# Performance work log

Measured on AMD Instinct MI355X. Metric: run time of the kernel, lower is better.

The kernel has to match this reference:

```python
import jax, jax.numpy as jnp
import numpy as np

T = 256        # number of time steps (len(ts))
B = 4096       # batch of independent ODE trajectories
D = 64         # data_size (state dim)
W = 256        # width_size
DT = 0.01      # time step


def setup_inputs() -> dict:
    key = jax.random.key(0)
    ks = jax.random.split(key, 9)
    ts = jnp.arange(T, dtype=jnp.float32) * DT
    y0 = jax.random.normal(ks[0], (B, D), dtype=jnp.float32)
    # MLP params: layers D->W, W->W, W->W, W->D (depth=3 hidden layers)
    def lin(k, out_d, in_d):
        return jax.random.normal(k, (out_d, in_d), dtype=jnp.float32) / np.float32(np.sqrt(in_d))
    w0 = lin(ks[1], W, D)
    b0 = jax.random.normal(ks[2], (W,), dtype=jnp.float32) * 0.01
    w1 = lin(ks[3], W, W)
    b1 = jax.random.normal(ks[4], (W,), dtype=jnp.float32) * 0.01
    w2 = lin(ks[5], W, W)
    b2 = jax.random.normal(ks[6], (W,), dtype=jnp.float32) * 0.01
    w3 = lin(ks[7], D, W)
    b3 = jax.random.normal(ks[8], (D,), dtype=jnp.float32) * 0.01
    return {"ts": ts, "y0": y0, "w0": w0, "b0": b0, "w1": w1, "b1": b1,
            "w2": w2, "b2": b2, "w3": w3, "b3": b3}


def reference(ts, y0, w0, b0, w1, b1, w2, b2, w3, b3):
    def mlp(y):  # y: [B, D] -> [B, D], softplus hidden activations
        h = jax.nn.softplus(y @ w0.T + b0)
        h = jax.nn.softplus(h @ w1.T + b1)
        h = jax.nn.softplus(h @ w2.T + b2)
        return h @ w3.T + b3

    dt = ts[1] - ts[0]

    def step(y, _):
        k1 = mlp(y)
        # NOTE: faithful to source: perturbations are 0.5*k1 and 0.75*k2 (no dt factor)
        k2 = mlp(y + 0.5 * k1)
        k3 = mlp(y + 0.75 * k2)
        y1 = (2.0 / 9.0 * k1 + 1.0 / 3.0 * k2 + 4.0 / 9.0 * k3) * dt + y
        return y1, y1

    _, ys = jax.lax.scan(step, y0, xs=None, length=ts.shape[0])
    return ys  # [T, B, D]
```

## Files before the change

kernel.cpp:

```cpp
#include <hip/hip_runtime.h>
#include <stdint.h>
#include <stddef.h>

constexpr int T_STEPS  = 256;
constexpr int B_ROWS   = 4096;
constexpr int D_DIM    = 64;
constexpr int W_DIM    = 256;
constexpr int ROWS_PB  = 16;
constexpr int NTHREADS = 512;

typedef __attribute__((ext_vector_type(8))) __bf16 bf16x8;
typedef __attribute__((ext_vector_type(8))) short  short8;
typedef __attribute__((ext_vector_type(4))) float  f32x4;

__device__ __forceinline__ unsigned f2bf_bits(float f) {
    union { float f; unsigned u; } v; v.f = f;
    return (v.u + 0x7FFFu + ((v.u >> 16) & 1u)) >> 16;
}

__device__ __forceinline__ uint32_t cvt_pk_bf16(float lo, float hi) {
    uint32_t r;
    asm("v_cvt_pk_bf16_f32 %0, %1, %2" : "=v"(r) : "v"(lo), "v"(hi));
    return r;
}

__device__ __forceinline__ float softplus_f(float x) {
    float e = __builtin_amdgcn_exp2f(-fabsf(x) * 1.44269504f);
    float l = __builtin_amdgcn_logf(1.0f + e);
    return fmaxf(x, 0.0f) + 0.69314718f * l;
}

__device__ __forceinline__ bf16x8 load_wfrag(const float* __restrict__ wg, int ldk,
                                             int f, int kcbase, int lg) {
    short8 s;
#pragma unroll
    for (int j = 0; j < 8; ++j) {
        const int k = kcbase + lg * 4 + (j >> 1) + ((j & 1) << 4);
        s[j] = (short)f2bf_bits(wg[(size_t)f * ldk + k]);
    }
    return __builtin_bit_cast(bf16x8, s);
}

template<int NKC>
__device__ __forceinline__ void mlp_layer(const uint32_t* __restrict__ srow,
                                          uint32_t* __restrict__ dst,
                                          const bf16x8* wf0, const bf16x8* wf1,
                                          float b0v, float b1v,
                                          int lr, int lg, int fbdw)
{
    const int swz = (lr & 7) << 2;
    f32x4 a0 = {b0v, b0v, b0v, b0v};
    f32x4 a1 = {b1v, b1v, b1v, b1v};
#pragma unroll
    for (int kc = 0; kc < NKC; ++kc) {
        const bf16x8 a = *reinterpret_cast<const bf16x8*>(srow + ((kc * 16 + lg * 4) ^ swz));
        a0 = __builtin_amdgcn_mfma_f32_16x16x32_bf16(a, wf0[kc], a0, 0, 0, 0);
        a1 = __builtin_amdgcn_mfma_f32_16x16x32_bf16(a, wf1[kc], a1, 0, 0, 0);
    }
#pragma unroll
    for (int j = 0; j < 4; ++j) {
        const int r = lg * 4 + j;
        dst[(size_t)r * 128 + ((fbdw + lr) ^ ((r & 7) << 2))] =
            cvt_pk_bf16(softplus_f(a0[j]), softplus_f(a1[j]));
    }
}

__global__ __launch_bounds__(NTHREADS, 2) void node_rk3_kernel(
    const float* __restrict__ ts,
    const float* __restrict__ y0,
    const float* __restrict__ w0, const float* __restrict__ b0,
    const float* __restrict__ w1, const float* __restrict__ b1,
    const float* __restrict__ w2, const float* __restrict__ b2,
    const float* __restrict__ w3, const float* __restrict__ b3,
    float* __restrict__ out)
{
    __shared__ __align__(16) uint32_t hs0[ROWS_PB][128];
    __shared__ __align__(16) uint32_t hs1[ROWS_PB][128];
    __shared__ __align__(16) uint32_t ybf[ROWS_PB][32];

    const int tid  = threadIdx.x;
    const int lane = tid & 63;
    const int wid  = tid >> 6;
    const int lr   = lane & 15;
    const int lg   = lane >> 4;
    const int row0 = blockIdx.x * ROWS_PB;
    const int fbdw = wid * 16;

    bf16x8 w0f[2][2], w1f[2][8], w2f[2][8], w3f[8];
#pragma unroll
    for (int nt = 0; nt < 2; ++nt) {
        const int f = wid * 32 + nt * 16 + lr;
#pragma unroll
        for (int kc = 0; kc < 2; ++kc) w0f[nt][kc] = load_wfrag(w0, D_DIM, f, kc * 32, lg);
#pragma unroll
        for (int kc = 0; kc < 8; ++kc) w1f[nt][kc] = load_wfrag(w1, W_DIM, f, kc * 32, lg);
#pragma unroll
        for (int kc = 0; kc < 8; ++kc) w2f[nt][kc] = load_wfrag(w2, W_DIM, f, kc * 32, lg);
    }
    const int f3 = (wid & 3) * 16;
#pragma unroll
    for (int kc = 0; kc < 8; ++kc) w3f[kc] = load_wfrag(w3, W_DIM, f3 + lr, kc * 32, lg);

    const float bA0 = b0[wid * 32 + lr], bB0 = b0[wid * 32 + 16 + lr];
    const float bA1 = b1[wid * 32 + lr], bB1 = b1[wid * 32 + 16 + lr];
    const float bA2 = b2[wid * 32 + lr], bB2 = b2[wid * 32 + 16 + lr];
    const float bv3 = b3[f3 + lr];

    const float dt = ts[1] - ts[0];

    float yreg[4], k1r[4], k2r[4];
#pragma unroll
    for (int j = 0; j < 4; ++j)
        yreg[j] = y0[(size_t)(row0 + lg * 4 + j) * D_DIM + f3 + lr];
#pragma unroll
    for (int j = 0; j < 4; ++j) { k1r[j] = 0.f; k2r[j] = 0.f; }

    for (int i = tid; i < ROWS_PB * 32; i += NTHREADS) {
        const int r = i >> 5, c32 = i & 31, kb = c32 >> 4, u = c32 & 15;
        const float* yr = y0 + (size_t)(row0 + r) * D_DIM;
        ybf[r][(kb * 16 + u) ^ ((r & 7) << 2)] = cvt_pk_bf16(yr[kb * 32 + u], yr[kb * 32 + 16 + u]);
    }
    __syncthreads();

    for (int t = 0; t < T_STEPS; ++t) {
#pragma unroll
        for (int c = 0; c < 3; ++c) {
            mlp_layer<2>(&ybf[lr][0], &hs0[0][0], w0f[0], w0f[1], bA0, bB0, lr, lg, fbdw);
            __syncthreads();
            mlp_layer<8>(&hs0[lr][0], &hs1[0][0], w1f[0], w1f[1], bA1, bB1, lr, lg, fbdw);
            __syncthreads();
            mlp_layer<8>(&hs1[lr][0], &hs0[0][0], w2f[0], w2f[1], bA2, bB2, lr, lg, fbdw);
            __syncthreads();
            if (wid < 4) {
                const int swz = (lr & 7) << 2;
                f32x4 acc = {bv3, bv3, bv3, bv3};
#pragma unroll
                for (int kc = 0; kc < 8; ++kc) {
                    const bf16x8 a = *reinterpret_cast<const bf16x8*>(&hs0[lr][(kc * 16 + lg * 4) ^ swz]);
                    acc = __builtin_amdgcn_mfma_f32_16x16x32_bf16(a, w3f[kc], acc, 0, 0, 0);
                }
                const int kb = wid >> 1, hi = wid & 1;
#pragma unroll
                for (int j = 0; j < 4; ++j) {
                    const int r = lg * 4 + j;
                    float v;
                    if (c == 0)      { k1r[j] = acc[j]; v = fmaf(0.5f,  acc[j], yreg[j]); }
                    else if (c == 1) { k2r[j] = acc[j]; v = fmaf(0.75f, acc[j], yreg[j]); }
                    else {
                        v = yreg[j] + dt * ((2.0f / 9.0f) * k1r[j]
                                          + (1.0f / 3.0f) * k2r[j]
                                          + (4.0f / 9.0f) * acc[j]);
                        yreg[j] = v;
                        out[((size_t)t * B_ROWS + row0 + r) * D_DIM + f3 + lr] = v;
                    }
                    uint16_t* p = (uint16_t*)&ybf[r][(kb * 16 + lr) ^ ((r & 7) << 2)];
                    p[hi] = (uint16_t)cvt_pk_bf16(v, v);
                }
            }
            __syncthreads();
        }
    }
}

extern "C" void kernel_launch(void* const* d_in, const int* in_sizes, int n_in,
                              void* d_out, int out_size, void* d_ws, size_t ws_size,
                              hipStream_t stream) {
    const float* ts = (const float*)d_in[0];
    const float* y0 = (const float*)d_in[1];
    const float* w0 = (const float*)d_in[2];
    const float* b0 = (const float*)d_in[3];
    const float* w1 = (const float*)d_in[4];
    const float* b1 = (const float*)d_in[5];
    const float* w2 = (const float*)d_in[6];
    const float* b2 = (const float*)d_in[7];
    const float* w3 = (const float*)d_in[8];
    const float* b3 = (const float*)d_in[9];
    float* out = (float*)d_out;

    hipLaunchKernelGGL(node_rk3_kernel,
                       dim3(B_ROWS / ROWS_PB), dim3(NTHREADS), 0, stream,
                       ts, y0, w0, b0, w1, b1, w2, b2, w3, b3, out);
}
```

Measured before the change: 1.671 ms.

## Fold log2e/ln2 into weights, pad LDS rows, defer output stores

Scales layer-0 weights and all hidden biases by log2(e), and w3 by ln2, so that softplus runs in the base-2 domain with no per-element multiplies. This relies on layers 1 and 2 being unaffected because the scaled activation and the scaled pre-activation cancel. XOR-swizzled LDS addressing is replaced by padded row strides (132/36) with precomputed pointers, which removes index arithmetic. Global output stores are deferred to the start of the next step to take them off the critical path, and weight loads are vectorized with float4. Changing the bf16 rounding of the scaled weights slightly alters numerics.

After: 1.399 ms. -16.3%, faster.

```diff
diff --git a/kernel.cpp b/kernel.cpp
--- a/kernel.cpp
+++ b/kernel.cpp
@@ -8,6 +8,12 @@
 constexpr int W_DIM    = 256;
 constexpr int ROWS_PB  = 16;
 constexpr int NTHREADS = 512;
+
+constexpr int HS_LD = 132;
+constexpr int YB_LD = 36;
+
+constexpr float LOG2E = 1.44269504088896f;
+constexpr float LN2   = 0.693147180559945f;
 
 typedef __attribute__((ext_vector_type(8))) __bf16 bf16x8;
 typedef __attribute__((ext_vector_type(8))) short  short8;
@@ -24,45 +30,40 @@
     return r;
 }
 
-__device__ __forceinline__ float softplus_f(float x) {
-    float e = __builtin_amdgcn_exp2f(-fabsf(x) * 1.44269504f);
-    float l = __builtin_amdgcn_logf(1.0f + e);
-    return fmaxf(x, 0.0f) + 0.69314718f * l;
+__device__ __forceinline__ float act_g(float u) {
+    float e = __builtin_amdgcn_exp2f(-fabsf(u));
+    return fmaxf(u, 0.0f) + __builtin_amdgcn_logf(1.0f + e);
 }
 
 __device__ __forceinline__ bf16x8 load_wfrag(const float* __restrict__ wg, int ldk,
-                                             int f, int kcbase, int lg) {
+                                             int f, int kcb, int lg, float scale) {
+    const float4 a = *reinterpret_cast<const float4*>(wg + (size_t)f * ldk + kcb + lg * 4);
+    const float4 b = *reinterpret_cast<const float4*>(wg + (size_t)f * ldk + kcb + 16 + lg * 4);
     short8 s;
-#pragma unroll
-    for (int j = 0; j < 8; ++j) {
-        const int k = kcbase + lg * 4 + (j >> 1) + ((j & 1) << 4);
-        s[j] = (short)f2bf_bits(wg[(size_t)f * ldk + k]);
-    }
+    s[0] = (short)f2bf_bits(a.x * scale); s[1] = (short)f2bf_bits(b.x * scale);
+    s[2] = (short)f2bf_bits(a.y * scale); s[3] = (short)f2bf_bits(b.y * scale);
+    s[4] = (short)f2bf_bits(a.z * scale); s[5] = (short)f2bf_bits(b.z * scale);
+    s[6] = (short)f2bf_bits(a.w * scale); s[7] = (short)f2bf_bits(b.w * scale);
     return __builtin_bit_cast(bf16x8, s);
 }
 
 template<int NKC>
-__device__ __forceinline__ void mlp_layer(const uint32_t* __restrict__ srow,
+__device__ __forceinline__ void mlp_layer(const uint32_t* __restrict__ src,
                                           uint32_t* __restrict__ dst,
                                           const bf16x8* wf0, const bf16x8* wf1,
-                                          float b0v, float b1v,
-                                          int lr, int lg, int fbdw)
+                                          float b0v, float b1v)
 {
-    const int swz = (lr & 7) << 2;
     f32x4 a0 = {b0v, b0v, b0v, b0v};
     f32x4 a1 = {b1v, b1v, b1v, b1v};
 #pragma unroll
     for (int kc = 0; kc < NKC; ++kc) {
-        const bf16x8 a = *reinterpret_cast<const bf16x8*>(srow + ((kc * 16 + lg * 4) ^ swz));
+        const bf16x8 a = *reinterpret_cast<const bf16x8*>(src + kc * 16);
         a0 = __builtin_amdgcn_mfma_f32_16x16x32_bf16(a, wf0[kc], a0, 0, 0, 0);
         a1 = __builtin_amdgcn_mfma_f32_16x16x32_bf16(a, wf1[kc], a1, 0, 0, 0);
     }
 #pragma unroll
-    for (int j = 0; j < 4; ++j) {
-        const int r = lg * 4 + j;
-        dst[(size_t)r * 128 + ((fbdw + lr) ^ ((r & 7) << 2))] =
-            cvt_pk_bf16(softplus_f(a0[j]), softplus_f(a1[j]));
-    }
+    for (int j = 0; j < 4; ++j)
+        dst[j * HS_LD] = cvt_pk_bf16(act_g(a0[j]), act_g(a1[j]));
 }
 
 __global__ __launch_bounds__(NTHREADS, 2) void node_rk3_kernel(
@@ -74,9 +75,9 @@
     const float* __restrict__ w3, const float* __restrict__ b3,
     float* __restrict__ out)
 {
-    __shared__ __align__(16) uint32_t hs0[ROWS_PB][128];
-    __shared__ __align__(16) uint32_t hs1[ROWS_PB][128];
-    __shared__ __align__(16) uint32_t ybf[ROWS_PB][32];
+    __shared__ __align__(16) uint32_t hs0[ROWS_PB][HS_LD];
+    __shared__ __align__(16) uint32_t hs1[ROWS_PB][HS_LD];
+    __shared__ __align__(16) uint32_t ybf[ROWS_PB][YB_LD];
 
     const int tid  = threadIdx.x;
     const int lane = tid & 63;
@@ -91,58 +92,68 @@
     for (int nt = 0; nt < 2; ++nt) {
         const int f = wid * 32 + nt * 16 + lr;
 #pragma unroll
-        for (int kc = 0; kc < 2; ++kc) w0f[nt][kc] = load_wfrag(w0, D_DIM, f, kc * 32, lg);
+        for (int kc = 0; kc < 2; ++kc) w0f[nt][kc] = load_wfrag(w0, D_DIM, f, kc * 32, lg, LOG2E);
 #pragma unroll
-        for (int kc = 0; kc < 8; ++kc) w1f[nt][kc] = load_wfrag(w1, W_DIM, f, kc * 32, lg);
+        for (int kc = 0; kc < 8; ++kc) w1f[nt][kc] = load_wfrag(w1, W_DIM, f, kc * 32, lg, 1.0f);
 #pragma unroll
-        for (int kc = 0; kc < 8; ++kc) w2f[nt][kc] = load_wfrag(w2, W_DIM, f, kc * 32, lg);
+        for (int kc = 0; kc < 8; ++kc) w2f[nt][kc] = load_wfrag(w2, W_DIM, f, kc * 32, lg, 1.0f);
     }
     const int f3 = (wid & 3) * 16;
 #pragma unroll
-    for (int kc = 0; kc < 8; ++kc) w3f[kc] = load_wfrag(w3, W_DIM, f3 + lr, kc * 32, lg);
+    for (int kc = 0; kc < 8; ++kc) w3f[kc] = load_wfrag(w3, W_DIM, f3 + lr, kc * 32, lg, LN2);
 
-    const float bA0 = b0[wid * 32 + lr], bB0 = b0[wid * 32 + 16 + lr];
-    const float bA1 = b1[wid * 32 + lr], bB1 = b1[wid * 32 + 16 + lr];
-    const float bA2 = b2[wid * 32 + lr], bB2 = b2[wid * 32 + 16 + lr];
+    const float bA0 = LOG2E * b0[wid * 32 + lr], bB0 = LOG2E * b0[wid * 32 + 16 + lr];
+    const float bA1 = LOG2E * b1[wid * 32 + lr], bB1 = LOG2E * b1[wid * 32 + 16 + lr];
+    const float bA2 = LOG2E * b2[wid * 32 + lr], bB2 = LOG2E * b2[wid * 32 + 16 + lr];
     const float bv3 = b3[f3 + lr];
 
     const float dt = ts[1] - ts[0];
 
-    float yreg[4], k1r[4], k2r[4];
+    const uint32_t* pA_y  = &ybf[lr][lg * 4];
+    const uint32_t* pA_h0 = &hs0[lr][lg * 4];
+    const uint32_t* pA_h1 = &hs1[lr][lg * 4];
+    uint32_t* pW_h0 = &hs0[lg * 4][fbdw + lr];
+    uint32_t* pW_h1 = &hs1[lg * 4][fbdw + lr];
+    const int kb = wid >> 1, hi = wid & 1;
+    uint16_t* pYW = (uint16_t*)&ybf[0][0] + ((size_t)(lg * 4) * YB_LD + kb * 16 + lr) * 2 + hi;
+
+    float yreg[4], k1r[4], k2r[4], vst[4];
 #pragma unroll
-    for (int j = 0; j < 4; ++j)
+    for (int j = 0; j < 4; ++j) {
         yreg[j] = y0[(size_t)(row0 + lg * 4 + j) * D_DIM + f3 + lr];
-#pragma unroll
-    for (int j = 0; j < 4; ++j) { k1r[j] = 0.f; k2r[j] = 0.f; }
+        k1r[j] = 0.f; k2r[j] = 0.f; vst[j] = 0.f;
+    }
 
     for (int i = tid; i < ROWS_PB * 32; i += NTHREADS) {
-        const int r = i >> 5, c32 = i & 31, kb = c32 >> 4, u = c32 & 15;
+        const int r = i >> 5, c32 = i & 31, kbi = c32 >> 4, u = c32 & 15;
         const float* yr = y0 + (size_t)(row0 + r) * D_DIM;
-        ybf[r][(kb * 16 + u) ^ ((r & 7) << 2)] = cvt_pk_bf16(yr[kb * 32 + u], yr[kb * 32 + 16 + u]);
+        ybf[r][kbi * 16 + u] = cvt_pk_bf16(yr[kbi * 32 + u], yr[kbi * 32 + 16 + u]);
     }
     __syncthreads();
 
     for (int t = 0; t < T_STEPS; ++t) {
+        if (wid < 4 && t > 0) {
+#pragma unroll
+            for (int j = 0; j < 4; ++j)
+                out[((size_t)(t - 1) * B_ROWS + row0 + lg * 4 + j) * D_DIM + f3 + lr] = vst[j];
+        }
 #pragma unroll
         for (int c = 0; c < 3; ++c) {
-            mlp_layer<2>(&ybf[lr][0], &hs0[0][0], w0f[0], w0f[1], bA0, bB0, lr, lg, fbdw);
+            mlp_layer<2>(pA_y,  pW_h0, w0f[0], w0f[1], bA0, bB0);
             __syncthreads();
-            mlp_layer<8>(&hs0[lr][0], &hs1[0][0], w1f[0], w1f[1], bA1, bB1, lr, lg, fbdw);
+            mlp_layer<8>(pA_h0, pW_h1, w1f[0], w1f[1], bA1, bB1);
             __syncthreads();
-            mlp_layer<8>(&hs1[lr][0], &hs0[0][0], w2f[0], w2f[1], bA2, bB2, lr, lg, fbdw);
+            mlp_layer<8>(pA_h1, pW_h0, w2f[0], w2f[1], bA2, bB2);
             __syncthreads();
             if (wid < 4) {
-                const int swz = (lr & 7) << 2;
                 f32x4 acc = {bv3, bv3, bv3, bv3};
 #pragma unroll
                 for (int kc = 0; kc < 8; ++kc) {
-                    const bf16x8 a = *reinterpret_cast<const bf16x8*>(&hs0[lr][(kc * 16 + lg * 4) ^ swz]);
+                    const bf16x8 a = *reinterpret_cast<const bf16x8*>(pA_h0 + kc * 16);
                     acc = __builtin_amdgcn_mfma_f32_16x16x32_bf16(a, w3f[kc], acc, 0, 0, 0);
                 }
-                const int kb = wid >> 1, hi = wid & 1;
 #pragma unroll
                 for (int j = 0; j < 4; ++j) {
-                    const int r = lg * 4 + j;
                     float v;
                     if (c == 0)      { k1r[j] = acc[j]; v = fmaf(0.5f,  acc[j], yreg[j]); }
                     else if (c == 1) { k2r[j] = acc[j]; v = fmaf(0.75f, acc[j], yreg[j]); }
@@ -151,14 +162,18 @@
                                           + (1.0f / 3.0f) * k2r[j]
                                           + (4.0f / 9.0f) * acc[j]);
                         yreg[j] = v;
-                        out[((size_t)t * B_ROWS + row0 + r) * D_DIM + f3 + lr] = v;
+                        vst[j]  = v;
                     }
-                    uint16_t* p = (uint16_t*)&ybf[r][(kb * 16 + lr) ^ ((r & 7) << 2)];
-                    p[hi] = (uint16_t)cvt_pk_bf16(v, v);
+                    pYW[j * YB_LD * 2] = (uint16_t)cvt_pk_bf16(v, v);
                 }
             }
             __syncthreads();
         }
+    }
+    if (wid < 4) {
+#pragma unroll
+        for (int j = 0; j < 4; ++j)
+            out[((size_t)(T_STEPS - 1) * B_ROWS + row0 + lg * 4 + j) * D_DIM + f3 + lr] = vst[j];
     }
 }
 
```
